# Kernel tuning notes

Measured on AMD Instinct MI355X. Metric: run time of the kernel, lower is better.

Reference implementation:

```python
import jax, jax.numpy as jnp
import numpy as np

C, M, G = 16, 64, 16            # hidden states, alphabet, n_gen
T, D = 64, 10                   # number of trees, depth (perfect binary)
N1 = 2 ** (D + 1) - 1           # nodes per tree (heap layout)
DIM = T * N1                    # total nodes = 131008
N_LEAVES = T * 2 ** D
_E = [T * 2 ** l for l in range(1, D + 1)]        # edges at each level l
_U = [T * 2 ** (l - 1) for l in range(1, D + 1)]  # unique parents at each level l
_EOFF = [0] + list(np.cumsum(_E))
_UOFF = [0] + list(np.cumsum(_U))


def _tree_structure():
    base = (np.arange(T) * N1)[:, None]
    pas, chs, ups = [], [], []
    for l in range(1, D + 1):
        ch = (np.arange(2 ** l - 1, 2 ** (l + 1) - 1)[None, :] + base).reshape(-1)
        pa = (ch % N1 - 1) // 2 + (ch // N1) * N1   # heap parent, global index
        up = (np.arange(2 ** (l - 1) - 1, 2 ** l - 1)[None, :] + base).reshape(-1)
        pas.append(pa); chs.append(ch); ups.append(up)
    return np.concatenate(pas), np.concatenate(chs), np.concatenate(ups)


def setup_inputs() -> dict:
    key = jax.random.key(0)
    k1, k2, k3, k4 = jax.random.split(key, 4)
    pa, ch, up = _tree_structure()
    leaves = (np.arange(2 ** D - 1, N1)[None, :] + (np.arange(T) * N1)[:, None]).reshape(-1)
    return {
        'x': jax.random.randint(k1, (DIM,), 0, M, dtype=jnp.int32),
        'leaves': jnp.asarray(leaves, jnp.int32),
        'trees_ind': jnp.asarray(np.repeat(np.arange(T), N1), jnp.int32),
        'parents_flat': jnp.asarray(pa, jnp.int32),
        'children_flat': jnp.asarray(ch, jnp.int32),
        'uparents_flat': jnp.asarray(up, jnp.int32),
        'inv_map': jnp.arange(DIM, dtype=jnp.int32),
        'lambda_A': jax.random.uniform(k2, (C, C, G), jnp.float32),
        'lambda_B': jax.random.uniform(k3, (C, M, G), jnp.float32),
        'lambda_Pi': jax.random.uniform(k4, (C, G), jnp.float32),
    }


def reference(x, leaves, trees_ind, parents_flat, children_flat, uparents_flat, inv_map,
              lambda_A, lambda_B, lambda_Pi):
    # softmax-normalized parameters (per generative model g)
    A = jax.nn.softmax(lambda_A, axis=0)    # (C,C,G)  transition, normalized over arrival state
    Bm = jax.nn.softmax(lambda_B, axis=1)   # (C,M,G)  emission over symbols
    Pi = jax.nn.softmax(lambda_Pi, axis=0)  # (C,G)    leaf prior

    beta = jnp.zeros((DIM, C, G), lambda_A.dtype)
    ll = jnp.zeros((DIM, G), lambda_A.dtype)

    # leaves: beta = Pi * B[:, x_leaf]
    b_leaf = jnp.transpose(Bm[:, x[inv_map[leaves]]], (1, 0, 2))  # (L,C,G)
    beta_leaf = Pi[None] * b_leaf
    nu = beta_leaf.sum(axis=1)                                    # (L,G)
    beta = beta.at[leaves].set(beta_leaf / nu[:, None, :])
    ll = ll.at[leaves].set(jnp.log(nu))

    # bottom-up over levels (static loop, D=10 iterations)
    for l in range(D, 0, -1):
        e0, e1 = _EOFF[l - 1], _EOFF[l]
        u0, u1 = _UOFF[l - 1], _UOFF[l]
        pa = parents_flat[e0:e1]
        ch = children_flat[e0:e1]
        up = uparents_flat[u0:u1]
        beta_ch = beta[ch]                                   # (E,C,G) gather
        t_beta_ch = jnp.einsum('ijg,ejg->eig', A, beta_ch)   # sum_j A[i,j,g]*beta_ch[e,j,g]
        t_sum = jax.ops.segment_sum(t_beta_ch, pa, num_segments=DIM)
        cnt = jax.ops.segment_sum(jnp.ones((pa.shape[0],), beta.dtype), pa, num_segments=DIM)
        t_beta_up = t_sum[up] / cnt[up][:, None, None]       # scatter-mean over children
        b_l = jnp.transpose(Bm[:, x[inv_map[up]]], (1, 0, 2))
        beta_l = b_l * t_beta_up
        nu = beta_l.sum(axis=1)
        beta = beta.at[up].set(beta_l / nu[:, None, :])
        ll = ll.at[up].set(jnp.log(nu))

    # per-tree log-likelihood: scatter-sum of node log nu over trees
    return jax.ops.segment_sum(ll, trees_ind, num_segments=T)  # (T,G)
```

## Files before the change

### kernel.cpp

```cpp
#include <hip/hip_runtime.h>


#define C_DIM 16
#define M_DIM 64
#define G_DIM 16
#define T_TREES 64
#define N1 2047
#define NBLOCKS (T_TREES * G_DIM)
#define BTS 20

__device__ __forceinline__ float4 f4add(float4 a, float4 b) {
    return make_float4(a.x + b.x, a.y + b.y, a.z + b.z, a.w + b.w);
}
__device__ __forceinline__ float4 f4mul(float4 a, float4 b) {
    return make_float4(a.x * b.x, a.y * b.y, a.z * b.z, a.w * b.w);
}
__device__ __forceinline__ float4 f4fma(float4 a, float4 b, float4 c) {
    return make_float4(fmaf(a.x, b.x, c.x), fmaf(a.y, b.y, c.y),
                       fmaf(a.z, b.z, c.z), fmaf(a.w, b.w, c.w));
}
__device__ __forceinline__ float hsum4(float4 a) { return a.x + a.y + a.z + a.w; }

__device__ __forceinline__ float matvec_bt(const float* __restrict__ A,
                                           const float* __restrict__ bt,
                                           const float4 sv[4], float4 bp[4])
{
    float nu = 0.f;
    #pragma unroll
    for (int h = 0; h < 2; ++h) {
        #pragma unroll
        for (int q = 2 * h; q < 2 * h + 2; ++q) {
            const float4 b4 = *(const float4*)(bt + 4 * q);
            float tr[4];
            #pragma unroll
            for (int r = 0; r < 4; ++r) {
                const float4* ar = (const float4*)(A + (4 * q + r) * 16);
                float4 m = f4mul(ar[0], sv[0]);
                m = f4fma(ar[1], sv[1], m);
                m = f4fma(ar[2], sv[2], m);
                m = f4fma(ar[3], sv[3], m);
                tr[r] = hsum4(m);
            }
            bp[q] = f4mul(make_float4(tr[0], tr[1], tr[2], tr[3]), b4);
            nu += hsum4(bp[q]);
        }
        __builtin_amdgcn_sched_barrier(0);
    }
    return nu;
}

__global__ __attribute__((amdgpu_flat_work_group_size(256, 256),
                          amdgpu_waves_per_eu(5)))
void htmm_fused(
    const int* __restrict__ x,
    const int* __restrict__ inv_map,
    const float* __restrict__ lA,
    const float* __restrict__ lB,
    const float* __restrict__ lPi,
    float* __restrict__ out)
{
    const int bid = blockIdx.x;
    const int tid = threadIdx.x;
    const int g = bid >> 6;
    const int t = bid & (T_TREES - 1);

    __shared__ __align__(16) unsigned char smem[32768];
    float* const sA   = (float*)(smem);
    float* const sBt  = (float*)(smem + 1024);
    float* const sPB  = (float*)(smem + 6144);
    float* const sLog = (float*)(smem + 11264);
    float* const sPi  = (float*)(smem + 11520);
    float* const buf1 = (float*)(smem + 6144);
    unsigned char* const xs = smem + 14336;
    float* const buf0 = (float*)(smem + 16384);
    float* const wsum = (float*)(smem + 32752);

    {
        const int base = t * N1;
        for (int i = tid; i < N1; i += 256)
            xs[i] = (unsigned char)x[inv_map[base + i]];
    }
    {
        int j = tid >> 4, i = tid & 15;
        float v = lA[(i * C_DIM + j) * G_DIM + g];
        float mx = v;
        #pragma unroll
        for (int m = 1; m < 16; m <<= 1) mx = fmaxf(mx, __shfl_xor(mx, m, 16));
        float e = __expf(v - mx);
        float s = e;
        #pragma unroll
        for (int m = 1; m < 16; m <<= 1) s += __shfl_xor(s, m, 16);
        sA[i * C_DIM + j] = e / s;
    }
    {
        int c = tid >> 4, l16 = tid & 15;
        float e0 = lB[(c * M_DIM + l16 +  0) * G_DIM + g];
        float e1 = lB[(c * M_DIM + l16 + 16) * G_DIM + g];
        float e2 = lB[(c * M_DIM + l16 + 32) * G_DIM + g];
        float e3 = lB[(c * M_DIM + l16 + 48) * G_DIM + g];
        float mx = fmaxf(fmaxf(e0, e1), fmaxf(e2, e3));
        #pragma unroll
        for (int m = 1; m < 16; m <<= 1) mx = fmaxf(mx, __shfl_xor(mx, m, 16));
        e0 = __expf(e0 - mx); e1 = __expf(e1 - mx);
        e2 = __expf(e2 - mx); e3 = __expf(e3 - mx);
        float s = e0 + e1 + e2 + e3;
        #pragma unroll
        for (int m = 1; m < 16; m <<= 1) s += __shfl_xor(s, m, 16);
        float inv = 1.f / s;
        sBt[(l16 +  0) * BTS + c] = e0 * inv;
        sBt[(l16 + 16) * BTS + c] = e1 * inv;
        sBt[(l16 + 32) * BTS + c] = e2 * inv;
        sBt[(l16 + 48) * BTS + c] = e3 * inv;
    }
    if (tid < C_DIM) {
        float v = lPi[tid * G_DIM + g];
        float mx = v;
        #pragma unroll
        for (int m = 1; m < 16; m <<= 1) mx = fmaxf(mx, __shfl_xor(mx, m, 16));
        float e = __expf(v - mx);
        float s = e;
        #pragma unroll
        for (int m = 1; m < 16; m <<= 1) s += __shfl_xor(s, m, 16);
        sPi[tid] = e / s;
    }
    __syncthreads();

    if (tid < M_DIM) {
        const int xv = tid;
        float pb[16]; float nu = 0.f;
        #pragma unroll
        for (int k = 0; k < 16; ++k) {
            pb[k] = sPi[k] * sBt[xv * BTS + k];
            nu += pb[k];
        }
        const float inv = 0.5f / nu;
        #pragma unroll
        for (int k = 0; k < 16; ++k) sPB[xv * BTS + k] = pb[k] * inv;
        sLog[xv] = __logf(nu);
    }
    __syncthreads();

    float ll = 0.f;

    {
        const int idx = tid;
        const int p8  = 255 + idx;
        float4 s8v[4];
        #pragma unroll
        for (int q = 0; q < 4; ++q) s8v[q] = make_float4(0.f, 0.f, 0.f, 0.f);

        #pragma unroll
        for (int c9 = 0; c9 < 2; ++c9) {
            const int p9 = 2 * p8 + 1 + c9;
            const int xl = xs[2 * p9 + 1], xr = xs[2 * p9 + 2];
            const float* pl = &sPB[xl * BTS];
            const float* pr = &sPB[xr * BTS];
            float4 s9v[4];
            #pragma unroll
            for (int q = 0; q < 4; ++q)
                s9v[q] = f4add(*(const float4*)(pl + 4*q), *(const float4*)(pr + 4*q));
            ll += sLog[xl] + sLog[xr];

            const int xv = xs[p9];
            float4 bp[4];
            float nu = matvec_bt(sA, &sBt[xv * BTS], s9v, bp);
            ll += __logf(nu);
            const float inv = 0.5f / nu;
            const float4 iv = make_float4(inv, inv, inv, inv);
            #pragma unroll
            for (int q = 0; q < 4; ++q) s8v[q] = f4fma(bp[q], iv, s8v[q]);
            __builtin_amdgcn_sched_barrier(0);
        }
        const int xv = xs[p8];
        float4 bp[4];
        float nu = matvec_bt(sA, &sBt[xv * BTS], s8v, bp);
        ll += __logf(nu);
        const float inv = 1.f / nu;
        #pragma unroll
        for (int q = 0; q < 4; ++q) {
            buf0[(4*q + 0) * 256 + idx] = bp[q].x * inv;
            buf0[(4*q + 1) * 256 + idx] = bp[q].y * inv;
            buf0[(4*q + 2) * 256 + idx] = bp[q].z * inv;
            buf0[(4*q + 3) * 256 + idx] = bp[q].w * inv;
        }
    }
    __syncthreads();

    if (tid < 128) {
        const int idx = tid;
        float4 sv[4];
        #pragma unroll
        for (int q = 0; q < 4; ++q) {
            float2 c0 = *(const float2*)(&buf0[(4*q + 0) * 256 + 2 * idx]);
            float2 c1 = *(const float2*)(&buf0[(4*q + 1) * 256 + 2 * idx]);
            float2 c2 = *(const float2*)(&buf0[(4*q + 2) * 256 + 2 * idx]);
            float2 c3 = *(const float2*)(&buf0[(4*q + 3) * 256 + 2 * idx]);
            sv[q] = make_float4(0.5f * (c0.x + c0.y), 0.5f * (c1.x + c1.y),
                                0.5f * (c2.x + c2.y), 0.5f * (c3.x + c3.y));
        }
        const int xv = xs[127 + idx];
        float4 bp[4];
        float nu = matvec_bt(sA, &sBt[xv * BTS], sv, bp);
        ll += __logf(nu);
        const float inv = 1.f / nu;
        #pragma unroll
        for (int q = 0; q < 4; ++q) {
            buf1[(4*q + 0) * 128 + idx] = bp[q].x * inv;
            buf1[(4*q + 1) * 128 + idx] = bp[q].y * inv;
            buf1[(4*q + 2) * 128 + idx] = bp[q].z * inv;
            buf1[(4*q + 3) * 128 + idx] = bp[q].w * inv;
        }
    }
    __syncthreads();

    if (tid < 64) {
        float* cur = buf1; int cs = 128;
        float* nxt = buf0; int ns = 256;
        for (int cnt2 = 64; cnt2 >= 1; cnt2 >>= 1) {
            if (tid < cnt2) {
                const int idx = tid;
                float4 sv[4];
                #pragma unroll
                for (int q = 0; q < 4; ++q) {
                    float2 c0 = *(const float2*)(&cur[(4*q + 0) * cs + 2 * idx]);
                    float2 c1 = *(const float2*)(&cur[(4*q + 1) * cs + 2 * idx]);
                    float2 c2 = *(const float2*)(&cur[(4*q + 2) * cs + 2 * idx]);
                    float2 c3 = *(const float2*)(&cur[(4*q + 3) * cs + 2 * idx]);
                    sv[q] = make_float4(0.5f * (c0.x + c0.y), 0.5f * (c1.x + c1.y),
                                        0.5f * (c2.x + c2.y), 0.5f * (c3.x + c3.y));
                }
                const int xv = xs[cnt2 - 1 + idx];
                float4 bp[4];
                float nu = matvec_bt(sA, &sBt[xv * BTS], sv, bp);
                ll += __logf(nu);
                const float inv = 1.f / nu;
                #pragma unroll
                for (int q = 0; q < 4; ++q) {
                    nxt[(4*q + 0) * ns + idx] = bp[q].x * inv;
                    nxt[(4*q + 1) * ns + idx] = bp[q].y * inv;
                    nxt[(4*q + 2) * ns + idx] = bp[q].z * inv;
                    nxt[(4*q + 3) * ns + idx] = bp[q].w * inv;
                }
            }
            asm volatile("s_waitcnt lgkmcnt(0)" ::: "memory");
            __builtin_amdgcn_wave_barrier();
            float* tp = cur; cur = nxt; nxt = tp;
            int ts = cs; cs = ns; ns = ts;
        }
    }

    float v = ll;
    #pragma unroll
    for (int off = 32; off > 0; off >>= 1) v += __shfl_down(v, off, 64);
    if ((tid & 63) == 0) wsum[tid >> 6] = v;
    __syncthreads();
    if (tid == 0) out[t * G_DIM + g] = wsum[0] + wsum[1] + wsum[2] + wsum[3];
}

extern "C" void kernel_launch(void* const* d_in, const int* in_sizes, int n_in,
                              void* d_out, int out_size, void* d_ws, size_t ws_size,
                              hipStream_t stream) {
    const int*   x       = (const int*)d_in[0];
    const int*   inv_map = (const int*)d_in[6];
    const float* lA      = (const float*)d_in[7];
    const float* lB      = (const float*)d_in[8];
    const float* lPi     = (const float*)d_in[9];
    float* out = (float*)d_out;

    htmm_fused<<<dim3(NBLOCKS), dim3(256), 0, stream>>>(
        x, inv_map, lA, lB, lPi, out);
}
```

Measured before the change: 112.5 us.

## Partition upper tree levels per wave to replace block barriers with wave barriers

Each of the four waves now owns a contiguous quarter of the subtree, so levels 7 down to 2 are processed within a wave using only an LDS wait and wave barrier instead of block-wide __syncthreads. Only the last two root levels need a block barrier and run on wave 0. The launch attributes also change from waves_per_eu(5) to launch_bounds(256,1), which alters the register and occupancy budget. Lane utilisation inside each wave drops, since at most 32 lanes per wave are active at these levels.

```diff
diff --git a/kernel.cpp b/kernel.cpp
--- a/kernel.cpp
+++ b/kernel.cpp
@@ -49,9 +49,7 @@
     return nu;
 }
 
-__global__ __attribute__((amdgpu_flat_work_group_size(256, 256),
-                          amdgpu_waves_per_eu(5)))
-void htmm_fused(
+__global__ __launch_bounds__(256, 1) void htmm_fused(
     const int* __restrict__ x,
     const int* __restrict__ inv_map,
     const float* __restrict__ lA,
@@ -63,6 +61,8 @@
     const int tid = threadIdx.x;
     const int g = bid >> 6;
     const int t = bid & (T_TREES - 1);
+    const int wv   = tid >> 6;
+    const int lane = tid & 63;
 
     __shared__ __align__(16) unsigned char smem[32768];
     float* const sA   = (float*)(smem);
@@ -142,6 +142,7 @@
 
     float ll = 0.f;
 
+
     {
         const int idx = tid;
         const int p8  = 255 + idx;
@@ -184,41 +185,80 @@
             buf0[(4*q + 3) * 256 + idx] = bp[q].w * inv;
         }
     }
+    asm volatile("s_waitcnt lgkmcnt(0)" ::: "memory");
+    __builtin_amdgcn_wave_barrier();
+
+    {
+        if (lane < 32) {
+            const int idx = 32 * wv + lane;
+            float4 sv[4];
+            #pragma unroll
+            for (int q = 0; q < 4; ++q) {
+                float2 c0 = *(const float2*)(&buf0[(4*q + 0) * 256 + 2 * idx]);
+                float2 c1 = *(const float2*)(&buf0[(4*q + 1) * 256 + 2 * idx]);
+                float2 c2 = *(const float2*)(&buf0[(4*q + 2) * 256 + 2 * idx]);
+                float2 c3 = *(const float2*)(&buf0[(4*q + 3) * 256 + 2 * idx]);
+                sv[q] = make_float4(0.5f * (c0.x + c0.y), 0.5f * (c1.x + c1.y),
+                                    0.5f * (c2.x + c2.y), 0.5f * (c3.x + c3.y));
+            }
+            const int xv = xs[127 + idx];
+            float4 bp[4];
+            float nu = matvec_bt(sA, &sBt[xv * BTS], sv, bp);
+            ll += __logf(nu);
+            const float inv = 1.f / nu;
+            #pragma unroll
+            for (int q = 0; q < 4; ++q) {
+                buf1[(4*q + 0) * 128 + idx] = bp[q].x * inv;
+                buf1[(4*q + 1) * 128 + idx] = bp[q].y * inv;
+                buf1[(4*q + 2) * 128 + idx] = bp[q].z * inv;
+                buf1[(4*q + 3) * 128 + idx] = bp[q].w * inv;
+            }
+        }
+        asm volatile("s_waitcnt lgkmcnt(0)" ::: "memory");
+        __builtin_amdgcn_wave_barrier();
+    }
+
+    float* cur = buf1; int cs = 128;
+    float* nxt = buf0; int ns = 256;
+    for (int cnt2 = 64; cnt2 >= 4; cnt2 >>= 1) {
+        const int c = cnt2 >> 2;
+        if (lane < c) {
+            const int idx = c * wv + lane;
+            float4 sv[4];
+            #pragma unroll
+            for (int q = 0; q < 4; ++q) {
+                float2 c0 = *(const float2*)(&cur[(4*q + 0) * cs + 2 * idx]);
+                float2 c1 = *(const float2*)(&cur[(4*q + 1) * cs + 2 * idx]);
+                float2 c2 = *(const float2*)(&cur[(4*q + 2) * cs + 2 * idx]);
+                float2 c3 = *(const float2*)(&cur[(4*q + 3) * cs + 2 * idx]);
+                sv[q] = make_float4(0.5f * (c0.x + c0.y), 0.5f * (c1.x + c1.y),
+                                    0.5f * (c2.x + c2.y), 0.5f * (c3.x + c3.y));
+            }
+            const int xv = xs[cnt2 - 1 + idx];
+            float4 bp[4];
+            float nu = matvec_bt(sA, &sBt[xv * BTS], sv, bp);
+            ll += __logf(nu);
+            const float inv = 1.f / nu;
+            #pragma unroll
+            for (int q = 0; q < 4; ++q) {
+                nxt[(4*q + 0) * ns + idx] = bp[q].x * inv;
+                nxt[(4*q + 1) * ns + idx] = bp[q].y * inv;
+                nxt[(4*q + 2) * ns + idx] = bp[q].z * inv;
+                nxt[(4*q + 3) * ns + idx] = bp[q].w * inv;
+            }
+        }
+        asm volatile("s_waitcnt lgkmcnt(0)" ::: "memory");
+        __builtin_amdgcn_wave_barrier();
+        float* tp = cur; cur = nxt; nxt = tp;
+        int ts = cs; cs = ns; ns = ts;
+    }
+
     __syncthreads();
 
-    if (tid < 128) {
-        const int idx = tid;
-        float4 sv[4];
-        #pragma unroll
-        for (int q = 0; q < 4; ++q) {
-            float2 c0 = *(const float2*)(&buf0[(4*q + 0) * 256 + 2 * idx]);
-            float2 c1 = *(const float2*)(&buf0[(4*q + 1) * 256 + 2 * idx]);
-            float2 c2 = *(const float2*)(&buf0[(4*q + 2) * 256 + 2 * idx]);
-            float2 c3 = *(const float2*)(&buf0[(4*q + 3) * 256 + 2 * idx]);
-            sv[q] = make_float4(0.5f * (c0.x + c0.y), 0.5f * (c1.x + c1.y),
-                                0.5f * (c2.x + c2.y), 0.5f * (c3.x + c3.y));
-        }
-        const int xv = xs[127 + idx];
-        float4 bp[4];
-        float nu = matvec_bt(sA, &sBt[xv * BTS], sv, bp);
-        ll += __logf(nu);
-        const float inv = 1.f / nu;
-        #pragma unroll
-        for (int q = 0; q < 4; ++q) {
-            buf1[(4*q + 0) * 128 + idx] = bp[q].x * inv;
-            buf1[(4*q + 1) * 128 + idx] = bp[q].y * inv;
-            buf1[(4*q + 2) * 128 + idx] = bp[q].z * inv;
-            buf1[(4*q + 3) * 128 + idx] = bp[q].w * inv;
-        }
-    }
-    __syncthreads();
-
-    if (tid < 64) {
-        float* cur = buf1; int cs = 128;
-        float* nxt = buf0; int ns = 256;
-        for (int cnt2 = 64; cnt2 >= 1; cnt2 >>= 1) {
-            if (tid < cnt2) {
-                const int idx = tid;
+    if (wv == 0) {
+        for (int cnt2 = 2; cnt2 >= 1; cnt2 >>= 1) {
+            if (lane < cnt2) {
+                const int idx = lane;
                 float4 sv[4];
                 #pragma unroll
                 for (int q = 0; q < 4; ++q) {
```

After: 124.6 us. +10.7%, slower.

## Precompute A-transformed leaf beta table per symbol to skip level-9 matvec

Applied to the files above, without the earlier changes.

Leaf betas depend only on the symbol, so the 64-entry table now stores A applied to the normalized leaf beta instead of the raw beta. Each level-9 node then just adds two precomputed child vectors and multiplies by emission, with no 16x16 matvec per node. By linearity the result is unchanged. Launch bounds also change from waves_per_eu(5) to __launch_bounds__(256,1), which relaxes the occupancy hint and register budget.

```diff
diff --git a/kernel.cpp b/kernel.cpp
--- a/kernel.cpp
+++ b/kernel.cpp
@@ -49,9 +49,7 @@
     return nu;
 }
 
-__global__ __attribute__((amdgpu_flat_work_group_size(256, 256),
-                          amdgpu_waves_per_eu(5)))
-void htmm_fused(
+__global__ __launch_bounds__(256, 1) void htmm_fused(
     const int* __restrict__ x,
     const int* __restrict__ inv_map,
     const float* __restrict__ lA,
@@ -135,8 +133,27 @@
         }
         const float inv = 0.5f / nu;
         #pragma unroll
-        for (int k = 0; k < 16; ++k) sPB[xv * BTS + k] = pb[k] * inv;
+        for (int k = 0; k < 16; ++k) pb[k] *= inv;
         sLog[xv] = __logf(nu);
+        const float4 pv0 = make_float4(pb[0],  pb[1],  pb[2],  pb[3]);
+        const float4 pv1 = make_float4(pb[4],  pb[5],  pb[6],  pb[7]);
+        const float4 pv2 = make_float4(pb[8],  pb[9],  pb[10], pb[11]);
+        const float4 pv3 = make_float4(pb[12], pb[13], pb[14], pb[15]);
+        float ta[16];
+        #pragma unroll
+        for (int i = 0; i < 16; ++i) {
+            const float4* ar = (const float4*)(sA + i * 16);
+            float4 m = f4mul(ar[0], pv0);
+            m = f4fma(ar[1], pv1, m);
+            m = f4fma(ar[2], pv2, m);
+            m = f4fma(ar[3], pv3, m);
+            ta[i] = hsum4(m);
+            if ((i & 3) == 3) __builtin_amdgcn_sched_barrier(0);
+        }
+        #pragma unroll
+        for (int q = 0; q < 4; ++q)
+            *(float4*)(&sPB[xv * BTS + 4 * q]) =
+                make_float4(ta[4*q], ta[4*q+1], ta[4*q+2], ta[4*q+3]);
     }
     __syncthreads();
 
@@ -153,18 +170,19 @@
         for (int c9 = 0; c9 < 2; ++c9) {
             const int p9 = 2 * p8 + 1 + c9;
             const int xl = xs[2 * p9 + 1], xr = xs[2 * p9 + 2];
-            const float* pl = &sPB[xl * BTS];
-            const float* pr = &sPB[xr * BTS];
-            float4 s9v[4];
+            const int xv = xs[p9];
+            const float* tl = &sPB[xl * BTS];
+            const float* tr = &sPB[xr * BTS];
+            const float* bt = &sBt[xv * BTS];
+            float4 bp[4]; float nu = 0.f;
             #pragma unroll
-            for (int q = 0; q < 4; ++q)
-                s9v[q] = f4add(*(const float4*)(pl + 4*q), *(const float4*)(pr + 4*q));
-            ll += sLog[xl] + sLog[xr];
-
-            const int xv = xs[p9];
-            float4 bp[4];
-            float nu = matvec_bt(sA, &sBt[xv * BTS], s9v, bp);
-            ll += __logf(nu);
+            for (int q = 0; q < 4; ++q) {
+                float4 tv = f4add(*(const float4*)(tl + 4*q),
+                                  *(const float4*)(tr + 4*q));
+                bp[q] = f4mul(tv, *(const float4*)(bt + 4*q));
+                nu += hsum4(bp[q]);
+            }
+            ll += sLog[xl] + sLog[xr] + __logf(nu);
             const float inv = 0.5f / nu;
             const float4 iv = make_float4(inv, inv, inv, inv);
             #pragma unroll
```

Measured after the change: 115.8 us. +2.9%, slower.
